# Kernel tuning notes

Measured on AMD Instinct MI355X. Metric: run time of the kernel, lower is better.

## Reference

```python
import jax, jax.numpy as jnp
import numpy as np

B, L, D = 4, 4096, 1024
H = 8
HD = D // H  # 128
SCALE = HD ** -0.5
RMS_EPS = 1.1920929e-07  # torch.finfo(float32).eps, nn.RMSNorm default eps=None


def rms_norm(x, g):
    ms = jnp.mean(jnp.square(x), axis=-1, keepdims=True)
    return x * jax.lax.rsqrt(ms + RMS_EPS) * g


def setup_inputs() -> dict:
    key = jax.random.key(0)
    ks = jax.random.split(key, 7)
    s = 0.02
    return {
        "x": jax.random.normal(ks[0], (B, L, D), dtype=jnp.float32),
        "W_qkv": jax.random.normal(ks[1], (D, 3 * D), dtype=jnp.float32) * s,
        "W_out": jax.random.normal(ks[2], (D, D), dtype=jnp.float32) * s,
        "g1": jnp.ones((D,), dtype=jnp.float32),
        "W_ff1": jax.random.normal(ks[3], (D, 4 * D), dtype=jnp.float32) * s,
        "W_ff2": jax.random.normal(ks[4], (4 * D, D), dtype=jnp.float32) * s,
        "g2": jnp.ones((D,), dtype=jnp.float32),
    }


def reference(x, W_qkv, W_out, g1, W_ff1, W_ff2, g2):
    b, l, _ = x.shape
    x_proj = x  # input_dim == latent_dim -> Identity
    qkv = (x_proj @ W_qkv).reshape(b, l, 3, H, HD)
    q, k, v = jnp.moveaxis(qkv, 2, 0)          # each [b, l, H, HD]
    q = jnp.transpose(q, (0, 2, 1, 3))          # [b, H, l, HD]
    k = jnp.transpose(k, (0, 2, 1, 3))
    v = jnp.transpose(v, (0, 2, 1, 3))
    if l <= 128:
        attn = jnp.einsum('bhqd,bhkd->bhqk', q, k) * SCALE
        attn = jax.nn.softmax(attn.astype(jnp.float32), axis=-1).astype(q.dtype)
        out = jnp.einsum('bhqk,bhkd->bhqd', attn, v)
    else:
        q = jax.nn.elu(q) + 1.0
        k = jax.nn.elu(k) + 1.0
        kv = jnp.einsum('bhld,bhlm->bhdm', k, v)            # [b,H,HD,HD]
        out = jnp.einsum('bhld,bhdm->bhlm', q, kv)          # [b,H,l,HD]
        k_sum = jnp.sum(k, axis=2, keepdims=True)           # [b,H,1,HD]
        normalizer = jnp.einsum('bhld,bhmd->bhlm', q, k_sum)  # [b,H,l,1]
        out = out / (normalizer + 1e-08)
    out = jnp.transpose(out, (0, 2, 1, 3)).reshape(b, l, D)
    out = out @ W_out  # dropout is identity (p=0 / eval)
    out = rms_norm(out + x_proj, g1)
    ffn = jax.nn.gelu(out @ W_ff1, approximate=False) @ W_ff2
    return rms_norm(ffn + out, g2)
```

## Files before the change

### kernel.cpp

```cpp
#include <hip/hip_runtime.h>
#include <hip/hip_bf16.h>
#include <math.h>

typedef __bf16 bf16;
typedef __attribute__((ext_vector_type(8))) __bf16 bf16x8;
typedef __attribute__((ext_vector_type(4))) __bf16 bf16x4;
typedef __attribute__((ext_vector_type(4))) float f32x4;

#define BB 4
#define LL 4096
#define DD 1024
#define HH 8
#define HDIM 128
#define MTOK 16384
#define DFF 4096

#define BM 128
#define BN 128
#define BK 32

__device__ __forceinline__ void gload_lds16(const bf16* g, bf16* l) {
  __builtin_amdgcn_global_load_lds(
      (const __attribute__((address_space(1))) void*)g,
      (__attribute__((address_space(3))) void*)l, 16, 0, 0);
}

__device__ __forceinline__ float elu1f(float v) {
  return v > 0.f ? v + 1.f : expf(v);
}
__device__ __forceinline__ float gelu_exact(float v) {
  return 0.5f * v * (1.f + erff(v * 0.70710678118654752f));
}

template <class EpiF>
__device__ __forceinline__ void gemm_bt_core(const bf16* __restrict__ A,
                                             const bf16* __restrict__ BT,
                                             int K, int m0, int n0, EpiF epi) {
  __shared__ bf16 As[BM * BK];
  __shared__ bf16 Bs[BN * BK];
  const int t = threadIdx.x;
  const int wv = t >> 6, lane = t & 63;
  const int fr = lane & 15, fg = lane >> 4;
  const int wm = (wv >> 1) * 64, wn = (wv & 1) * 64;

  const bf16* ga = A + (size_t)(m0 + (t >> 2)) * K + ((t & 3) << 3);
  const bf16* gb = BT + (size_t)(n0 + (t >> 2)) * K + ((t & 3) << 3);
  bf16* asw = As + wv * 512;
  bf16* bsw = Bs + wv * 512;

  f32x4 acc[4][4];
#pragma unroll
  for (int i = 0; i < 4; ++i)
#pragma unroll
    for (int j = 0; j < 4; ++j) acc[i][j] = (f32x4){0.f, 0.f, 0.f, 0.f};

  for (int k0 = 0; k0 < K; k0 += BK) {
    gload_lds16(ga + k0, asw);
    gload_lds16(ga + k0 + (size_t)64 * K, asw + 2048);
    gload_lds16(gb + k0, bsw);
    gload_lds16(gb + k0 + (size_t)64 * K, bsw + 2048);
    __syncthreads();
    bf16x8 af[4], bfr[4];
#pragma unroll
    for (int i = 0; i < 4; ++i)
      af[i] = *(const bf16x8*)(As + (wm + i * 16 + fr) * BK + fg * 8);
#pragma unroll
    for (int j = 0; j < 4; ++j)
      bfr[j] = *(const bf16x8*)(Bs + (wn + j * 16 + fr) * BK + fg * 8);
#pragma unroll
    for (int i = 0; i < 4; ++i)
#pragma unroll
      for (int j = 0; j < 4; ++j)
        acc[i][j] = __builtin_amdgcn_mfma_f32_16x16x32_bf16(af[i], bfr[j],
                                                            acc[i][j], 0, 0, 0);
    __syncthreads();
  }
#pragma unroll
  for (int i = 0; i < 4; ++i)
#pragma unroll
    for (int j = 0; j < 4; ++j)
#pragma unroll
      for (int r = 0; r < 4; ++r)
        epi(m0 + wm + i * 16 + fg * 4 + r, n0 + wn + j * 16 + fr, acc[i][j][r]);
}

__global__ __launch_bounds__(256) void k_conv_bf16(const float* __restrict__ xin,
                                                   bf16* __restrict__ xo) {
  int i = blockIdx.x * 256 + threadIdx.x;
  float4 v = ((const float4*)xin)[i];
  bf16x4 o = {(bf16)v.x, (bf16)v.y, (bf16)v.z, (bf16)v.w};
  *(bf16x4*)(xo + (size_t)i * 4) = o;
}

__global__ void k_transpose_w(const float* __restrict__ W, bf16* __restrict__ WTo,
                              int K, int N) {
  __shared__ float tile[32][33];
  int n0 = blockIdx.x * 32, k0 = blockIdx.y * 32;
  int x = threadIdx.x, y = threadIdx.y;
#pragma unroll
  for (int j = 0; j < 4; ++j)
    tile[y + 8 * j][x] = W[(size_t)(k0 + y + 8 * j) * N + n0 + x];
  __syncthreads();
#pragma unroll
  for (int j = 0; j < 4; ++j)
    WTo[(size_t)(n0 + y + 8 * j) * K + k0 + x] = (bf16)tile[x][y + 8 * j];
}

__global__ __launch_bounds__(256) void k_gemm_qkv(const bf16* __restrict__ xb,
                                                  const bf16* __restrict__ WT,
                                                  bf16* __restrict__ Q,
                                                  bf16* __restrict__ KT,
                                                  bf16* __restrict__ VT) {
  int m0 = blockIdx.y * BM, n0 = blockIdx.x * BN;
  gemm_bt_core(xb, WT, DD, m0, n0, [=](int r, int c, float v) {
    int b = r >> 12, l = r & (LL - 1);
    int which = c >> 10, cw = c & 1023, h = cw >> 7, d = cw & 127;
    size_t bh = (size_t)(b * HH + h);
    if (which == 0) {
      Q[(bh * LL + l) * HDIM + d] = (bf16)elu1f(v);
    } else if (which == 1) {
      KT[(bh * HDIM + d) * LL + l] = (bf16)elu1f(v);
    } else {
      VT[(bh * HDIM + d) * LL + l] = (bf16)v;
    }
  });
}

__global__ __launch_bounds__(256) void k_kv(const bf16* __restrict__ KT,
                                            const bf16* __restrict__ VT,
                                            bf16* __restrict__ kvT) {
  int bh = blockIdx.x;
  const bf16* A = KT + (size_t)bh * HDIM * LL;
  const bf16* Bt = VT + (size_t)bh * HDIM * LL;
  bf16* o = kvT + (size_t)bh * HDIM * HDIM;
  gemm_bt_core(A, Bt, LL, 0, 0,
               [=](int r, int c, float v) { o[c * HDIM + r] = (bf16)v; });
}

__global__ __launch_bounds__(256) void k_ksum(const bf16* __restrict__ KT,
                                              float* __restrict__ ksum) {
  int row = blockIdx.x;
  const bf16* p = KT + (size_t)row * LL;
  int t = threadIdx.x;
  bf16x8 v0 = *(const bf16x8*)(p + t * 16);
  bf16x8 v1 = *(const bf16x8*)(p + t * 16 + 8);
  float s = 0.f;
#pragma unroll
  for (int i = 0; i < 8; ++i) s += (float)v0[i] + (float)v1[i];
  for (int off = 32; off > 0; off >>= 1) s += __shfl_down(s, off);
  __shared__ float wpart[4];
  int lane = t & 63, wv = t >> 6;
  if (lane == 0) wpart[wv] = s;
  __syncthreads();
  if (t == 0) ksum[row] = wpart[0] + wpart[1] + wpart[2] + wpart[3];
}

__global__ __launch_bounds__(256) void k_attn_out(const bf16* __restrict__ Q,
                                                  const bf16* __restrict__ kvT,
                                                  const float* __restrict__ ksum,
                                                  bf16* __restrict__ attn) {
  const int bh = blockIdx.x, m0 = blockIdx.y * BM;
  const int b = bh >> 3, h = bh & 7;
  const bf16* A = Q + (size_t)bh * LL * HDIM;
  const bf16* Bt = kvT + (size_t)bh * HDIM * HDIM;
  __shared__ bf16 As[BM * BK];
  __shared__ bf16 Bs[BN * BK];
  __shared__ float ksum_s[HDIM];
  __shared__ float norm_s[BM];
  const int t = threadIdx.x, wv = t >> 6, lane = t & 63;
  const int fr = lane & 15, fg = lane >> 4;
  const int wm = (wv >> 1) * 64, wn = (wv & 1) * 64;
  if (t < HDIM) ksum_s[t] = ksum[bh * HDIM + t];
  const bf16* ga = A + (size_t)(m0 + (t >> 2)) * HDIM + ((t & 3) << 3);
  const bf16* gb = Bt + (size_t)(t >> 2) * HDIM + ((t & 3) << 3);
  bf16* asw = As + wv * 512;
  bf16* bsw = Bs + wv * 512;
  f32x4 acc[4][4];
#pragma unroll
  for (int i = 0; i < 4; ++i)
#pragma unroll
    for (int j = 0; j < 4; ++j) acc[i][j] = (f32x4){0.f, 0.f, 0.f, 0.f};
  float nacc = 0.f;
  for (int k0 = 0; k0 < HDIM; k0 += BK) {
    gload_lds16(ga + k0, asw);
    gload_lds16(ga + k0 + 64 * HDIM, asw + 2048);
    gload_lds16(gb + k0, bsw);
    gload_lds16(gb + k0 + 64 * HDIM, bsw + 2048);
    __syncthreads();
    bf16x8 af[4], bfr[4];
#pragma unroll
    for (int i = 0; i < 4; ++i)
      af[i] = *(const bf16x8*)(As + (wm + i * 16 + fr) * BK + fg * 8);
#pragma unroll
    for (int j = 0; j < 4; ++j)
      bfr[j] = *(const bf16x8*)(Bs + (wn + j * 16 + fr) * BK + fg * 8);
#pragma unroll
    for (int i = 0; i < 4; ++i)
#pragma unroll
      for (int j = 0; j < 4; ++j)
        acc[i][j] = __builtin_amdgcn_mfma_f32_16x16x32_bf16(af[i], bfr[j],
                                                            acc[i][j], 0, 0, 0);
    if (t < BM) {
#pragma unroll
      for (int j = 0; j < BK; ++j) nacc += (float)As[t * BK + j] * ksum_s[k0 + j];
    }
    __syncthreads();
  }
  if (t < BM) norm_s[t] = nacc;
  __syncthreads();
#pragma unroll
  for (int i = 0; i < 4; ++i)
#pragma unroll
    for (int j = 0; j < 4; ++j)
#pragma unroll
      for (int r = 0; r < 4; ++r) {
        int rl = wm + i * 16 + fg * 4 + r;
        int c = wn + j * 16 + fr;
        float denom = norm_s[rl] + 1e-8f;
        attn[((size_t)b * LL + m0 + rl) * DD + h * HDIM + c] =
            (bf16)(acc[i][j][r] / denom);
      }
}

__global__ __launch_bounds__(256) void k_gemm_wout(const bf16* __restrict__ attn,
                                                   const bf16* __restrict__ WT,
                                                   const float* __restrict__ x,
                                                   bf16* __restrict__ z) {
  int m0 = blockIdx.y * BM, n0 = blockIdx.x * BN;
  gemm_bt_core(attn, WT, DD, m0, n0, [=](int r, int c, float v) {
    size_t idx = (size_t)r * DD + c;
    z[idx] = (bf16)(v + x[idx]);
  });
}

__global__ __launch_bounds__(256) void k_gemm_ff1(const bf16* __restrict__ y1,
                                                  const bf16* __restrict__ WT,
                                                  bf16* __restrict__ hbuf) {
  int m0 = blockIdx.y * BM, n0 = blockIdx.x * BN;
  gemm_bt_core(y1, WT, DD, m0, n0, [=](int r, int c, float v) {
    hbuf[(size_t)r * DFF + c] = (bf16)gelu_exact(v);
  });
}

__global__ __launch_bounds__(256) void k_gemm_ff2(const bf16* __restrict__ hbuf,
                                                  const bf16* __restrict__ WT,
                                                  const bf16* __restrict__ y1,
                                                  bf16* __restrict__ z2) {
  int m0 = blockIdx.y * BM, n0 = blockIdx.x * BN;
  gemm_bt_core(hbuf, WT, DFF, m0, n0, [=](int r, int c, float v) {
    size_t idx = (size_t)r * DD + c;
    z2[idx] = (bf16)(v + (float)y1[idx]);
  });
}

template <typename OUT>
__global__ __launch_bounds__(256) void k_rmsnorm(const bf16* __restrict__ zin,
                                                 const float* __restrict__ g,
                                                 OUT* __restrict__ y) {
  const int row = blockIdx.x, t = threadIdx.x;
  const bf16* zr = zin + (size_t)row * DD;
  bf16x4 v = *(const bf16x4*)(zr + t * 4);
  float f0 = (float)v[0], f1 = (float)v[1], f2 = (float)v[2], f3 = (float)v[3];
  float ss = f0 * f0 + f1 * f1 + f2 * f2 + f3 * f3;
  for (int off = 32; off > 0; off >>= 1) ss += __shfl_down(ss, off);
  __shared__ float wsum[4];
  __shared__ float stot;
  int lane = t & 63, wv = t >> 6;
  if (lane == 0) wsum[wv] = ss;
  __syncthreads();
  if (t == 0) stot = wsum[0] + wsum[1] + wsum[2] + wsum[3];
  __syncthreads();
  float scale = rsqrtf(stot * (1.f / DD) + 1.1920929e-7f);
  size_t base = (size_t)row * DD + t * 4;
  y[base + 0] = (OUT)(f0 * scale * g[t * 4 + 0]);
  y[base + 1] = (OUT)(f1 * scale * g[t * 4 + 1]);
  y[base + 2] = (OUT)(f2 * scale * g[t * 4 + 2]);
  y[base + 3] = (OUT)(f3 * scale * g[t * 4 + 3]);
}

extern "C" void kernel_launch(void* const* d_in, const int* in_sizes, int n_in,
                              void* d_out, int out_size, void* d_ws, size_t ws_size,
                              hipStream_t stream) {
  (void)in_sizes; (void)n_in; (void)out_size; (void)ws_size;
  const float* x    = (const float*)d_in[0];
  const float* Wqkv = (const float*)d_in[1];
  const float* Wout = (const float*)d_in[2];
  const float* g1   = (const float*)d_in[3];
  const float* Wff1 = (const float*)d_in[4];
  const float* Wff2 = (const float*)d_in[5];
  const float* g2   = (const float*)d_in[6];
  float* out = (float*)d_out;

  char* ws = (char*)d_ws;
  const size_t MB = 1ull << 20;
  bf16* WqkvT = (bf16*)(ws + 0);
  bf16* WoutT = (bf16*)(ws + 6 * MB);
  bf16* Wff1T = (bf16*)(ws + 8 * MB);
  bf16* Wff2T = (bf16*)(ws + 16 * MB);
  bf16* xb    = (bf16*)(ws + 24 * MB);
  bf16* Q     = (bf16*)(ws + 56 * MB);
  bf16* KT    = (bf16*)(ws + 88 * MB);
  bf16* VT    = (bf16*)(ws + 120 * MB);
  bf16* attn  = xb;
  bf16* hbuf  = (bf16*)(ws + 24 * MB);
  bf16* kvT   = (bf16*)(ws + 152 * MB);
  float* ksum = (float*)(ws + 153 * MB);
  bf16* z     = (bf16*)(ws + 154 * MB);
  bf16* z2    = z;
  bf16* y1    = (bf16*)(ws + 186 * MB);

  k_conv_bf16<<<16384, 256, 0, stream>>>(x, xb);
  dim3 tb(32, 8);
  k_transpose_w<<<dim3(3072 / 32, 1024 / 32), tb, 0, stream>>>(Wqkv, WqkvT, 1024, 3072);
  k_transpose_w<<<dim3(1024 / 32, 1024 / 32), tb, 0, stream>>>(Wout, WoutT, 1024, 1024);
  k_transpose_w<<<dim3(4096 / 32, 1024 / 32), tb, 0, stream>>>(Wff1, Wff1T, 1024, 4096);
  k_transpose_w<<<dim3(1024 / 32, 4096 / 32), tb, 0, stream>>>(Wff2, Wff2T, 4096, 1024);

  k_gemm_qkv<<<dim3(3072 / BN, MTOK / BM), 256, 0, stream>>>(xb, WqkvT, Q, KT, VT);
  k_kv<<<32, 256, 0, stream>>>(KT, VT, kvT);
  k_ksum<<<4096, 256, 0, stream>>>(KT, ksum);
  k_attn_out<<<dim3(32, LL / BM), 256, 0, stream>>>(Q, kvT, ksum, attn);
  k_gemm_wout<<<dim3(1024 / BN, MTOK / BM), 256, 0, stream>>>(attn, WoutT, x, z);
  k_rmsnorm<bf16><<<MTOK, 256, 0, stream>>>(z, g1, y1);
  k_gemm_ff1<<<dim3(4096 / BN, MTOK / BM), 256, 0, stream>>>(y1, Wff1T, hbuf);
  k_gemm_ff2<<<dim3(1024 / BN, MTOK / BM), 256, 0, stream>>>(hbuf, Wff2T, y1, z2);
  k_rmsnorm<float><<<MTOK, 256, 0, stream>>>(z2, g2, out);
}
```

Baseline: 919.0 us.

## Use 256x256 double-buffered swizzled GEMM core and split-K kv reduction

Replaces the 128x128 single-buffered GEMM used for the QKV, Wout, FF1 and FF2 projections with a 256x256 tile, 512-thread kernel. The new kernel double-buffers 128KB of LDS with an XOR-swizzled layout, hand-places waitcnt/barriers and raises wave priority around the MFMA blocks. It also remaps workgroup IDs across XCDs for better L2 locality. The per-head K^T V product is split into 8 K-chunks plus a reduction kernel, so 256 blocks run instead of 32. The aim is more data reuse, load/compute overlap and occupancy, at the cost of heavy LDS use and a temporary fp32 partial buffer.

```diff
diff --git a/kernel.cpp b/kernel.cpp
--- a/kernel.cpp
+++ b/kernel.cpp
@@ -15,10 +15,6 @@
 #define MTOK 16384
 #define DFF 4096
 
-#define BM 128
-#define BN 128
-#define BK 32
-
 __device__ __forceinline__ void gload_lds16(const bf16* g, bf16* l) {
   __builtin_amdgcn_global_load_lds(
       (const __attribute__((address_space(1))) void*)g,
@@ -33,86 +29,123 @@
 }
 
 template <class EpiF>
-__device__ __forceinline__ void gemm_bt_core(const bf16* __restrict__ A,
+__device__ __forceinline__ void gemm256_core(const bf16* __restrict__ A,
                                              const bf16* __restrict__ BT,
                                              int K, int m0, int n0, EpiF epi) {
-  __shared__ bf16 As[BM * BK];
-  __shared__ bf16 Bs[BN * BK];
+  __shared__ __align__(16) char sm[131072];
   const int t = threadIdx.x;
-  const int wv = t >> 6, lane = t & 63;
+  const int wid = t >> 6, lane = t & 63;
   const int fr = lane & 15, fg = lane >> 4;
-  const int wm = (wv >> 1) * 64, wn = (wv & 1) * 64;
-
-  const bf16* ga = A + (size_t)(m0 + (t >> 2)) * K + ((t & 3) << 3);
-  const bf16* gb = BT + (size_t)(n0 + (t >> 2)) * K + ((t & 3) << 3);
-  bf16* asw = As + wv * 512;
-  bf16* bsw = Bs + wv * 512;
-
-  f32x4 acc[4][4];
-#pragma unroll
-  for (int i = 0; i < 4; ++i)
+  const int wm = wid >> 2, wn = wid & 3;
+  const int NT = K >> 6;
+
+  const int q0 = wid * 1024 + lane * 16;
+  const int q1 = q0 + 8192;
+  const int L0 = q0 ^ (((q0 >> 9) & 1) << 5);
+  const int L1 = q1 ^ (((q1 >> 9) & 1) << 5);
+  const bf16* ga0 = A + (size_t)(m0 + (L0 >> 6)) * K + ((L0 & 63) >> 1);
+  const bf16* ga1 = A + (size_t)(m0 + (L1 >> 6)) * K + ((L1 & 63) >> 1);
+  const bf16* gb0 = BT + (size_t)(n0 + (L0 >> 6)) * K + ((L0 & 63) >> 1);
+  const bf16* gb1 = BT + (size_t)(n0 + (L1 >> 6)) * K + ((L1 & 63) >> 1);
+  char* ld_w = sm + wid * 1024;
+
+#define STAGE_(bufb, isB, kk, kt)                                           \
+  do {                                                                      \
+    char* d_ = ld_w + (bufb) * 65536 + (isB) * 32768 + (kk) * 16384;        \
+    const bf16* s0_ = ((isB) ? gb0 : ga0) + (kt) * 64 + (kk) * 32;          \
+    const bf16* s1_ = ((isB) ? gb1 : ga1) + (kt) * 64 + (kk) * 32;          \
+    gload_lds16(s0_, (bf16*)d_);                                            \
+    gload_lds16(s1_, (bf16*)(d_ + 8192));                                   \
+  } while (0)
+
+  f32x4 acc[8][4];
+#pragma unroll
+  for (int i = 0; i < 8; ++i)
 #pragma unroll
     for (int j = 0; j < 4; ++j) acc[i][j] = (f32x4){0.f, 0.f, 0.f, 0.f};
-
-  for (int k0 = 0; k0 < K; k0 += BK) {
-    gload_lds16(ga + k0, asw);
-    gload_lds16(ga + k0 + (size_t)64 * K, asw + 2048);
-    gload_lds16(gb + k0, bsw);
-    gload_lds16(gb + k0 + (size_t)64 * K, bsw + 2048);
-    __syncthreads();
-    bf16x8 af[4], bfr[4];
-#pragma unroll
-    for (int i = 0; i < 4; ++i)
-      af[i] = *(const bf16x8*)(As + (wm + i * 16 + fr) * BK + fg * 8);
+  bf16x8 bfr[4];
+
+#define PHASE_(bufb, MH, KK, LOADB, doStage, sB, sIsB, sKk, sKt, VMW)       \
+  do {                                                                      \
+    bf16x8 af[4];                                                           \
+    _Pragma("unroll") for (int i = 0; i < 4; ++i) {                         \
+      int r_ = wm * 128 + (MH) * 64 + i * 16 + fr;                          \
+      int by_ = (bufb) * 65536 + (KK) * 16384 + r_ * 64 + fg * 16;          \
+      by_ ^= (r_ & 8) << 2;                                                 \
+      af[i] = *(const bf16x8*)(sm + by_);                                   \
+    }                                                                       \
+    if (LOADB) {                                                            \
+      _Pragma("unroll") for (int j = 0; j < 4; ++j) {                       \
+        int rn_ = wn * 64 + j * 16 + fr;                                    \
+        int by_ =                                                           \
+            (bufb) * 65536 + 32768 + (KK) * 16384 + rn_ * 64 + fg * 16;     \
+        by_ ^= (rn_ & 8) << 2;                                              \
+        bfr[j] = *(const bf16x8*)(sm + by_);                                \
+      }                                                                     \
+    }                                                                       \
+    if (doStage) STAGE_(sB, sIsB, sKk, sKt);                                \
+    if ((VMW) == 6) asm volatile("s_waitcnt vmcnt(6)" ::: "memory");        \
+    else if ((VMW) == 0) asm volatile("s_waitcnt vmcnt(0)" ::: "memory");   \
+    asm volatile("s_barrier" ::: "memory");                                 \
+    asm volatile("s_waitcnt lgkmcnt(0)" ::: "memory");                      \
+    __builtin_amdgcn_sched_barrier(0);                                      \
+    __builtin_amdgcn_s_setprio(1);                                          \
+    _Pragma("unroll") for (int i = 0; i < 4; ++i)                           \
+        _Pragma("unroll") for (int j = 0; j < 4; ++j) acc[(MH)*4 + i][j] =  \
+        __builtin_amdgcn_mfma_f32_16x16x32_bf16(af[i], bfr[j],              \
+                                                acc[(MH)*4 + i][j], 0, 0, 0); \
+    __builtin_amdgcn_s_setprio(0);                                          \
+    asm volatile("s_barrier" ::: "memory");                                 \
+  } while (0)
+
+  STAGE_(0, 0, 0, 0);
+  STAGE_(0, 1, 0, 0);
+  STAGE_(0, 0, 1, 0);
+  STAGE_(0, 1, 1, 0);
+  STAGE_(1, 0, 0, 1);
+  STAGE_(1, 1, 0, 1);
+  STAGE_(1, 0, 1, 1);
+  asm volatile("s_waitcnt vmcnt(6)" ::: "memory");
+  asm volatile("s_barrier" ::: "memory");
+
+  for (int T = 0; T < NT; ++T) {
+    const int bufb = T & 1, nb = bufb ^ 1;
+    const bool s1 = (T + 1 < NT);
+    const bool s2 = (T + 2 < NT);
+    const int vmw = s2 ? 6 : (s1 ? 0 : -1);
+    PHASE_(bufb, 0, 0, true, s1, nb, 1, 1, T + 1, -1);
+    PHASE_(bufb, 1, 0, false, s2, bufb, 0, 0, T + 2, -1);
+    PHASE_(bufb, 0, 1, true, s2, bufb, 1, 0, T + 2, -1);
+    PHASE_(bufb, 1, 1, false, s2, bufb, 0, 1, T + 2, vmw);
+  }
+#undef PHASE_
+#undef STAGE_
+
+#pragma unroll
+  for (int i = 0; i < 8; ++i)
 #pragma unroll
     for (int j = 0; j < 4; ++j)
-      bfr[j] = *(const bf16x8*)(Bs + (wn + j * 16 + fr) * BK + fg * 8);
-#pragma unroll
-    for (int i = 0; i < 4; ++i)
-#pragma unroll
-      for (int j = 0; j < 4; ++j)
-        acc[i][j] = __builtin_amdgcn_mfma_f32_16x16x32_bf16(af[i], bfr[j],
-                                                            acc[i][j], 0, 0, 0);
-    __syncthreads();
-  }
-#pragma unroll
-  for (int i = 0; i < 4; ++i)
-#pragma unroll
-    for (int j = 0; j < 4; ++j)
 #pragma unroll
       for (int r = 0; r < 4; ++r)
-        epi(m0 + wm + i * 16 + fg * 4 + r, n0 + wn + j * 16 + fr, acc[i][j][r]);
-}
-
-__global__ __launch_bounds__(256) void k_conv_bf16(const float* __restrict__ xin,
-                                                   bf16* __restrict__ xo) {
-  int i = blockIdx.x * 256 + threadIdx.x;
-  float4 v = ((const float4*)xin)[i];
-  bf16x4 o = {(bf16)v.x, (bf16)v.y, (bf16)v.z, (bf16)v.w};
-  *(bf16x4*)(xo + (size_t)i * 4) = o;
-}
-
-__global__ void k_transpose_w(const float* __restrict__ W, bf16* __restrict__ WTo,
-                              int K, int N) {
-  __shared__ float tile[32][33];
-  int n0 = blockIdx.x * 32, k0 = blockIdx.y * 32;
-  int x = threadIdx.x, y = threadIdx.y;
-#pragma unroll
-  for (int j = 0; j < 4; ++j)
-    tile[y + 8 * j][x] = W[(size_t)(k0 + y + 8 * j) * N + n0 + x];
-  __syncthreads();
-#pragma unroll
-  for (int j = 0; j < 4; ++j)
-    WTo[(size_t)(n0 + y + 8 * j) * K + k0 + x] = (bf16)tile[x][y + 8 * j];
-}
-
-__global__ __launch_bounds__(256) void k_gemm_qkv(const bf16* __restrict__ xb,
-                                                  const bf16* __restrict__ WT,
-                                                  bf16* __restrict__ Q,
-                                                  bf16* __restrict__ KT,
-                                                  bf16* __restrict__ VT) {
-  int m0 = blockIdx.y * BM, n0 = blockIdx.x * BN;
-  gemm_bt_core(xb, WT, DD, m0, n0, [=](int r, int c, float v) {
+        epi(m0 + wm * 128 + i * 16 + fg * 4 + r, n0 + wn * 64 + j * 16 + fr,
+            acc[i][j][r]);
+}
+
+__device__ __forceinline__ void tile_of(int Nt, int& mt, int& nt) {
+  int nwg = gridDim.x, bid = blockIdx.x;
+  int wg = (bid & 7) * (nwg >> 3) + (bid >> 3);
+  mt = wg / Nt;
+  nt = wg - mt * Nt;
+}
+
+__global__ __launch_bounds__(512, 2) void k256_qkv(const bf16* __restrict__ xb,
+                                                   const bf16* __restrict__ WT,
+                                                   bf16* __restrict__ Q,
+                                                   bf16* __restrict__ KT,
+                                                   bf16* __restrict__ VT, int Nt) {
+  int mt, nt;
+  tile_of(Nt, mt, nt);
+  gemm256_core(xb, WT, DD, mt * 256, nt * 256, [=](int r, int c, float v) {
     int b = r >> 12, l = r & (LL - 1);
     int which = c >> 10, cw = c & 1023, h = cw >> 7, d = cw & 127;
     size_t bh = (size_t)(b * HH + h);
@@ -126,15 +159,138 @@
   });
 }
 
-__global__ __launch_bounds__(256) void k_kv(const bf16* __restrict__ KT,
-                                            const bf16* __restrict__ VT,
-                                            bf16* __restrict__ kvT) {
-  int bh = blockIdx.x;
-  const bf16* A = KT + (size_t)bh * HDIM * LL;
-  const bf16* Bt = VT + (size_t)bh * HDIM * LL;
-  bf16* o = kvT + (size_t)bh * HDIM * HDIM;
-  gemm_bt_core(A, Bt, LL, 0, 0,
-               [=](int r, int c, float v) { o[c * HDIM + r] = (bf16)v; });
+__global__ __launch_bounds__(512, 2) void k256_wout(const bf16* __restrict__ attn,
+                                                    const bf16* __restrict__ WT,
+                                                    const float* __restrict__ x,
+                                                    bf16* __restrict__ z, int Nt) {
+  int mt, nt;
+  tile_of(Nt, mt, nt);
+  gemm256_core(attn, WT, DD, mt * 256, nt * 256, [=](int r, int c, float v) {
+    size_t idx = (size_t)r * DD + c;
+    z[idx] = (bf16)(v + x[idx]);
+  });
+}
+
+__global__ __launch_bounds__(512, 2) void k256_ff1(const bf16* __restrict__ y1,
+                                                   const bf16* __restrict__ WT,
+                                                   bf16* __restrict__ hbuf, int Nt) {
+  int mt, nt;
+  tile_of(Nt, mt, nt);
+  gemm256_core(y1, WT, DD, mt * 256, nt * 256, [=](int r, int c, float v) {
+    hbuf[(size_t)r * DFF + c] = (bf16)gelu_exact(v);
+  });
+}
+
+__global__ __launch_bounds__(512, 2) void k256_ff2(const bf16* __restrict__ hbuf,
+                                                   const bf16* __restrict__ WT,
+                                                   const bf16* __restrict__ y1,
+                                                   bf16* __restrict__ z2, int Nt) {
+  int mt, nt;
+  tile_of(Nt, mt, nt);
+  gemm256_core(hbuf, WT, DFF, mt * 256, nt * 256, [=](int r, int c, float v) {
+    size_t idx = (size_t)r * DD + c;
+    z2[idx] = (bf16)(v + (float)y1[idx]);
+  });
+}
+
+#define BM 128
+#define BN 128
+#define BK 32
+
+template <class EpiF>
+__device__ __forceinline__ void gemm_bt_core(const bf16* __restrict__ A,
+                                             const bf16* __restrict__ BT,
+                                             int K, int Klen, int m0, int n0,
+                                             EpiF epi) {
+  __shared__ bf16 As[BM * BK];
+  __shared__ bf16 Bs[BN * BK];
+  const int t = threadIdx.x;
+  const int wv = t >> 6, lane = t & 63;
+  const int fr = lane & 15, fg = lane >> 4;
+  const int wm = (wv >> 1) * 64, wn = (wv & 1) * 64;
+
+  const bf16* ga = A + (size_t)(m0 + (t >> 2)) * K + ((t & 3) << 3);
+  const bf16* gb = BT + (size_t)(n0 + (t >> 2)) * K + ((t & 3) << 3);
+  bf16* asw = As + wv * 512;
+  bf16* bsw = Bs + wv * 512;
+
+  f32x4 acc[4][4];
+#pragma unroll
+  for (int i = 0; i < 4; ++i)
+#pragma unroll
+    for (int j = 0; j < 4; ++j) acc[i][j] = (f32x4){0.f, 0.f, 0.f, 0.f};
+
+  for (int k0 = 0; k0 < Klen; k0 += BK) {
+    gload_lds16(ga + k0, asw);
+    gload_lds16(ga + k0 + (size_t)64 * K, asw + 2048);
+    gload_lds16(gb + k0, bsw);
+    gload_lds16(gb + k0 + (size_t)64 * K, bsw + 2048);
+    __syncthreads();
+    bf16x8 af[4], bfrg[4];
+#pragma unroll
+    for (int i = 0; i < 4; ++i)
+      af[i] = *(const bf16x8*)(As + (wm + i * 16 + fr) * BK + fg * 8);
+#pragma unroll
+    for (int j = 0; j < 4; ++j)
+      bfrg[j] = *(const bf16x8*)(Bs + (wn + j * 16 + fr) * BK + fg * 8);
+#pragma unroll
+    for (int i = 0; i < 4; ++i)
+#pragma unroll
+      for (int j = 0; j < 4; ++j)
+        acc[i][j] = __builtin_amdgcn_mfma_f32_16x16x32_bf16(af[i], bfrg[j],
+                                                            acc[i][j], 0, 0, 0);
+    __syncthreads();
+  }
+#pragma unroll
+  for (int i = 0; i < 4; ++i)
+#pragma unroll
+    for (int j = 0; j < 4; ++j)
+#pragma unroll
+      for (int r = 0; r < 4; ++r)
+        epi(m0 + wm + i * 16 + fg * 4 + r, n0 + wn + j * 16 + fr, acc[i][j][r]);
+}
+
+__global__ __launch_bounds__(256) void k_conv_bf16(const float* __restrict__ xin,
+                                                   bf16* __restrict__ xo) {
+  int i = blockIdx.x * 256 + threadIdx.x;
+  float4 v = ((const float4*)xin)[i];
+  bf16x4 o = {(bf16)v.x, (bf16)v.y, (bf16)v.z, (bf16)v.w};
+  *(bf16x4*)(xo + (size_t)i * 4) = o;
+}
+
+__global__ void k_transpose_w(const float* __restrict__ W, bf16* __restrict__ WTo,
+                              int K, int N) {
+  __shared__ float tile[32][33];
+  int n0 = blockIdx.x * 32, k0 = blockIdx.y * 32;
+  int x = threadIdx.x, y = threadIdx.y;
+#pragma unroll
+  for (int j = 0; j < 4; ++j)
+    tile[y + 8 * j][x] = W[(size_t)(k0 + y + 8 * j) * N + n0 + x];
+  __syncthreads();
+#pragma unroll
+  for (int j = 0; j < 4; ++j)
+    WTo[(size_t)(n0 + y + 8 * j) * K + k0 + x] = (bf16)tile[x][y + 8 * j];
+}
+
+__global__ __launch_bounds__(256) void k_kv_split(const bf16* __restrict__ KT,
+                                                  const bf16* __restrict__ VT,
+                                                  float* __restrict__ pbuf) {
+  int c = blockIdx.x >> 5;
+  int bh = blockIdx.x & 31;
+  const bf16* A = KT + (size_t)bh * HDIM * LL + c * 512;
+  const bf16* Bt = VT + (size_t)bh * HDIM * LL + c * 512;
+  float* o = pbuf + ((size_t)c * 32 + bh) * 16384;
+  gemm_bt_core(A, Bt, LL, 512, 0, 0,
+               [=](int r, int cc, float v) { o[cc * HDIM + r] = v; });
+}
+
+__global__ __launch_bounds__(256) void k_kv_reduce(const float* __restrict__ pbuf,
+                                                   bf16* __restrict__ kvT) {
+  int i = blockIdx.x * 256 + threadIdx.x;
+  float s = 0.f;
+#pragma unroll
+  for (int c = 0; c < 8; ++c) s += pbuf[(size_t)c * 524288 + i];
+  kvT[i] = (bf16)s;
 }
 
 __global__ __launch_bounds__(256) void k_ksum(const bf16* __restrict__ KT,
@@ -187,18 +343,18 @@
     gload_lds16(gb + k0, bsw);
     gload_lds16(gb + k0 + 64 * HDIM, bsw + 2048);
     __syncthreads();
-    bf16x8 af[4], bfr[4];
+    bf16x8 af[4], bfrg[4];
 #pragma unroll
     for (int i = 0; i < 4; ++i)
       af[i] = *(const bf16x8*)(As + (wm + i * 16 + fr) * BK + fg * 8);
 #pragma unroll
     for (int j = 0; j < 4; ++j)
-      bfr[j] = *(const bf16x8*)(Bs + (wn + j * 16 + fr) * BK + fg * 8);
+      bfrg[j] = *(const bf16x8*)(Bs + (wn + j * 16 + fr) * BK + fg * 8);
 #pragma unroll
     for (int i = 0; i < 4; ++i)
 #pragma unroll
       for (int j = 0; j < 4; ++j)
-        acc[i][j] = __builtin_amdgcn_mfma_f32_16x16x32_bf16(af[i], bfr[j],
+        acc[i][j] = __builtin_amdgcn_mfma_f32_16x16x32_bf16(af[i], bfrg[j],
                                                             acc[i][j], 0, 0, 0);
     if (t < BM) {
 #pragma unroll
@@ -220,37 +376,6 @@
         attn[((size_t)b * LL + m0 + rl) * DD + h * HDIM + c] =
             (bf16)(acc[i][j][r] / denom);
       }
-}
-
-__global__ __launch_bounds__(256) void k_gemm_wout(const bf16* __restrict__ attn,
-                                                   const bf16* __restrict__ WT,
-                                                   const float* __restrict__ x,
-                                                   bf16* __restrict__ z) {
-  int m0 = blockIdx.y * BM, n0 = blockIdx.x * BN;
-  gemm_bt_core(attn, WT, DD, m0, n0, [=](int r, int c, float v) {
-    size_t idx = (size_t)r * DD + c;
-    z[idx] = (bf16)(v + x[idx]);
-  });
-}
-
-__global__ __launch_bounds__(256) void k_gemm_ff1(const bf16* __restrict__ y1,
-                                                  const bf16* __restrict__ WT,
-                                                  bf16* __restrict__ hbuf) {
-  int m0 = blockIdx.y * BM, n0 = blockIdx.x * BN;
-  gemm_bt_core(y1, WT, DD, m0, n0, [=](int r, int c, float v) {
-    hbuf[(size_t)r * DFF + c] = (bf16)gelu_exact(v);
-  });
-}
-
-__global__ __launch_bounds__(256) void k_gemm_ff2(const bf16* __restrict__ hbuf,
-                                                  const bf16* __restrict__ WT,
-                                                  const bf16* __restrict__ y1,
-                                                  bf16* __restrict__ z2) {
-  int m0 = blockIdx.y * BM, n0 = blockIdx.x * BN;
-  gemm_bt_core(hbuf, WT, DFF, m0, n0, [=](int r, int c, float v) {
-    size_t idx = (size_t)r * DD + c;
-    z2[idx] = (bf16)(v + (float)y1[idx]);
-  });
 }
 
 template <typename OUT>
@@ -301,6 +426,7 @@
   bf16* Q     = (bf16*)(ws + 56 * MB);
   bf16* KT    = (bf16*)(ws + 88 * MB);
   bf16* VT    = (bf16*)(ws + 120 * MB);
+  float* pbuf = (float*)(ws + 24 * MB);
   bf16* attn  = xb;
   bf16* hbuf  = (bf16*)(ws + 24 * MB);
   bf16* kvT   = (bf16*)(ws + 152 * MB);
@@ -316,13 +442,18 @@
   k_transpose_w<<<dim3(4096 / 32, 1024 / 32), tb, 0, stream>>>(Wff1, Wff1T, 1024, 4096);
   k_transpose_w<<<dim3(1024 / 32, 4096 / 32), tb, 0, stream>>>(Wff2, Wff2T, 4096, 1024);
 
-  k_gemm_qkv<<<dim3(3072 / BN, MTOK / BM), 256, 0, stream>>>(xb, WqkvT, Q, KT, VT);
-  k_kv<<<32, 256, 0, stream>>>(KT, VT, kvT);
+  k256_qkv<<<(MTOK / 256) * (3072 / 256), 512, 0, stream>>>(xb, WqkvT, Q, KT, VT,
+                                                            3072 / 256);
+  k_kv_split<<<256, 256, 0, stream>>>(KT, VT, pbuf);
+  k_kv_reduce<<<2048, 256, 0, stream>>>(pbuf, kvT);
   k_ksum<<<4096, 256, 0, stream>>>(KT, ksum);
   k_attn_out<<<dim3(32, LL / BM), 256, 0, stream>>>(Q, kvT, ksum, attn);
-  k_gemm_wout<<<dim3(1024 / BN, MTOK / BM), 256, 0, stream>>>(attn, WoutT, x, z);
+  k256_wout<<<(MTOK / 256) * (1024 / 256), 512, 0, stream>>>(attn, WoutT, x, z,
+                                                             1024 / 256);
   k_rmsnorm<bf16><<<MTOK, 256, 0, stream>>>(z, g1, y1);
-  k_gemm_ff1<<<dim3(4096 / BN, MTOK / BM), 256, 0, stream>>>(y1, Wff1T, hbuf);
-  k_gemm_ff2<<<dim3(1024 / BN, MTOK / BM), 256, 0, stream>>>(hbuf, Wff2T, y1, z2);
+  k256_ff1<<<(MTOK / 256) * (4096 / 256), 512, 0, stream>>>(y1, Wff1T, hbuf,
+                                                            4096 / 256);
+  k256_ff2<<<(MTOK / 256) * (1024 / 256), 512, 0, stream>>>(hbuf, Wff2T, y1, z2,
+                                                            1024 / 256);
   k_rmsnorm<float><<<MTOK, 256, 0, stream>>>(z2, g2, out);
 }
```

Result: faster. 773.9 us (-15.8%).
